# Performance work log

Hardware: AMD Instinct MI355X
Metric: run time of the kernel (lower is better)

Reference implementation:

```python
import jax, jax.numpy as jnp
import numpy as np

N_NODES = 50000
N_EDGES = 800000
D_IN, D_HID, D_OUT = 64, 128, 64


def _glorot(key, fan_in, fan_out):
    lim = (6.0 / (fan_in + fan_out)) ** 0.5
    return jax.random.uniform(key, (fan_in, fan_out), jnp.float32, -lim, lim)


def setup_inputs() -> dict:
    key = jax.random.key(0)
    ks = jax.random.split(key, 10)
    x = jax.random.normal(ks[0], (N_NODES, D_IN), jnp.float32)
    edge_index = jax.random.randint(ks[1], (2, N_EDGES), 0, N_NODES, jnp.int64)
    # GINConv1 MLP: Linear(D_IN->D_HID), ReLU, Linear(D_HID->D_HID)
    W1a = _glorot(ks[2], D_IN, D_HID); b1a = jnp.zeros((D_HID,), jnp.float32)
    W1b = _glorot(ks[3], D_HID, D_HID); b1b = jnp.zeros((D_HID,), jnp.float32)
    # GINConv2 MLP: Linear(D_HID->D_HID), ReLU, Linear(D_HID->D_OUT)
    W2a = _glorot(ks[4], D_HID, D_HID); b2a = jnp.zeros((D_HID,), jnp.float32)
    W2b = _glorot(ks[5], D_HID, D_OUT); b2b = jnp.zeros((D_OUT,), jnp.float32)
    return {"x": x, "edge_index": edge_index,
            "W1a": W1a, "b1a": b1a, "W1b": W1b, "b1b": b1b,
            "W2a": W2a, "b2a": b2a, "W2b": W2b, "b2b": b2b}


def _gin_conv(x, src, dst, Wa, ba, Wb, bb):
    # GIN aggregation (eps = 0): h_i = x_i + sum_{j in N(i)} x_j
    msgs = x[src]                                   # [E, d] gather
    agg = jax.ops.segment_sum(msgs, dst, num_segments=x.shape[0])  # [N, d]
    h = x + agg
    # 2-layer MLP
    h = jax.nn.relu(h @ Wa + ba)
    return h @ Wb + bb


def reference(x, edge_index, W1a, b1a, W1b, b1b, W2a, b2a, W2b, b2b):
    src, dst = edge_index[0], edge_index[1]
    h = jax.nn.relu(_gin_conv(x, src, dst, W1a, b1a, W1b, b1b))
    h = jax.nn.relu(_gin_conv(h, src, dst, W2a, b2a, W2b, b2b))
    return h
```

## Files before the change

kernel.cpp:

```cpp
#include <hip/hip_runtime.h>

#define N_NODES 50000
#define N_EDGES 800000

typedef __attribute__((ext_vector_type(8))) short short8;
typedef __attribute__((ext_vector_type(4))) float floatx4;

static __device__ __forceinline__ unsigned short f2b(float f) {
    unsigned int u = __float_as_uint(f);
    unsigned int r = u + 0x7fffu + ((u >> 16) & 1u);
    return (unsigned short)(r >> 16);
}
static __device__ __forceinline__ unsigned int pk(float a, float b) {
    return (unsigned)f2b(a) | ((unsigned)f2b(b) << 16);
}
static __device__ __forceinline__ float blo(unsigned int u) {
    return __uint_as_float(u << 16);
}
static __device__ __forceinline__ float bhi(unsigned int u) {
    return __uint_as_float(u & 0xffff0000u);
}

static __device__ __forceinline__ void acc4(float* f, uint4 v0, uint4 v1,
                                            uint4 v2, uint4 v3) {
    f[0] += (blo(v0.x) + blo(v1.x)) + (blo(v2.x) + blo(v3.x));
    f[1] += (bhi(v0.x) + bhi(v1.x)) + (bhi(v2.x) + bhi(v3.x));
    f[2] += (blo(v0.y) + blo(v1.y)) + (blo(v2.y) + blo(v3.y));
    f[3] += (bhi(v0.y) + bhi(v1.y)) + (bhi(v2.y) + bhi(v3.y));
    f[4] += (blo(v0.z) + blo(v1.z)) + (blo(v2.z) + blo(v3.z));
    f[5] += (bhi(v0.z) + bhi(v1.z)) + (bhi(v2.z) + bhi(v3.z));
    f[6] += (blo(v0.w) + blo(v1.w)) + (blo(v2.w) + blo(v3.w));
    f[7] += (bhi(v0.w) + bhi(v1.w)) + (bhi(v2.w) + bhi(v3.w));
}

__global__ void hist_rank_kernel(const int* __restrict__ dst,
                                 int* __restrict__ deg, int* __restrict__ rank,
                                 int n) {
    int i = blockIdx.x * blockDim.x + threadIdx.x;
    if (i < n) rank[i] = atomicAdd(&deg[dst[i]], 1);
}

__global__ __launch_bounds__(1024) void offsets_kernel(
    const int* __restrict__ deg, int* __restrict__ offpd,
    int* __restrict__ gcount, unsigned short* __restrict__ nbr, int n) {
    __shared__ int s[1024];
    __shared__ int base;
    const int tid = threadIdx.x;
    const int i = blockIdx.x * 1024 + tid;
    const int d = (i < n) ? deg[i] : 0;
    const int pd = (d + 3) & ~3;
    s[tid] = pd;
    __syncthreads();
    for (int o = 1; o < 1024; o <<= 1) {
        int t = (tid >= o) ? s[tid - o] : 0;
        __syncthreads();
        s[tid] += t;
        __syncthreads();
    }
    if (tid == 1023) base = atomicAdd(gcount, s[1023]);
    __syncthreads();
    const int excl = base + s[tid] - pd;
    if (i < n) {
        offpd[i] = (excl << 10) | pd;
        for (int k = d; k < pd; ++k) nbr[excl + k] = (unsigned short)N_NODES;
    }
}

__global__ void fill_kernel(const int* __restrict__ src,
                            const int* __restrict__ dst,
                            const int* __restrict__ rank,
                            const int* __restrict__ offpd,
                            unsigned short* __restrict__ nbr, int n) {
    int i = blockIdx.x * blockDim.x + threadIdx.x;
    if (i < n) nbr[(offpd[dst[i]] >> 10) + rank[i]] = (unsigned short)src[i];
}

__global__ __launch_bounds__(256) void prep_kernel(
    const float* __restrict__ W1a, const float* __restrict__ W1b,
    const float* __restrict__ W2a, const float* __restrict__ W2b,
    const float* __restrict__ x, unsigned short* __restrict__ W1aT,
    unsigned short* __restrict__ W1bT, unsigned short* __restrict__ W2aT,
    unsigned short* __restrict__ W2bT, unsigned short* __restrict__ xb,
    unsigned short* __restrict__ h, int* __restrict__ deg,
    int* __restrict__ gcount) {
    int i = blockIdx.x * 256 + threadIdx.x;
    if (i < 8192) {
        int n = i >> 6, k = i & 63;
        W1aT[i] = f2b(W1a[k * 128 + n]);
    } else if (i < 24576) {
        int j = i - 8192, n = j >> 7, k = j & 127;
        W1bT[j] = f2b(W1b[k * 128 + n]);
    } else if (i < 40960) {
        int j = i - 24576, n = j >> 7, k = j & 127;
        W2aT[j] = f2b(W2a[k * 128 + n]);
    } else if (i < 49152) {
        int j = i - 40960, n = j >> 7, k = j & 127;
        W2bT[j] = f2b(W2b[k * 64 + n]);
    } else if (i < 49152 + N_NODES * 16) {
        int j = i - 49152;
        float4 v = ((const float4*)x)[j];
        uint2 o;
        o.x = pk(v.x, v.y);
        o.y = pk(v.z, v.w);
        ((uint2*)xb)[j] = o;
    } else if (i < 49152 + N_NODES * 16 + N_NODES) {
        int j = i - (49152 + N_NODES * 16);
        deg[j] = 0;
        if (j == 0) *gcount = 0;
    } else {
        int j = i - (49152 + N_NODES * 16 + N_NODES);
        uint4 z = {0u, 0u, 0u, 0u};
        if (j < 8)
            ((uint4*)(xb + (size_t)N_NODES * 64))[j] = z;
        else if (j < 24)
            ((uint4*)(h + (size_t)N_NODES * 128))[j - 8] = z;
    }
}

template <int DIN, int DH, int DOUT, bool OUT_BF16>
__global__ __launch_bounds__(256) void gin_fused_kernel(
    const unsigned short* __restrict__ xin, const int* __restrict__ offpd,
    const unsigned short* __restrict__ nbr,
    const unsigned short* __restrict__ WaT, const float* __restrict__ ba,
    const unsigned short* __restrict__ WbT, const float* __restrict__ bb,
    void* __restrict__ outp, int n_rows) {
    constexpr int ROWS = 64;
    constexpr int PASSES = DIN / 32;
    constexpr int RS = DIN / 8;
    constexpr int SA = DIN + 16;
    constexpr int SH = DH + 16;
    __shared__ __attribute__((aligned(16))) unsigned short tA[ROWS * SA];
    __shared__ __attribute__((aligned(16))) unsigned short hidA[ROWS * SH];

    const int tid = threadIdx.x;
    const int row0 = blockIdx.x * ROWS;
    const int grp = tid >> 2;
    const int c = tid & 3;
    const int node = row0 + grp;

    int lo = 0, hi = 0;
    if (node < n_rows) {
        const int v = offpd[node];
        lo = v >> 10;
        hi = lo + (v & 1023);
    }

    for (int q = 0; q < PASSES; ++q) {
        float f[8] = {0.f, 0.f, 0.f, 0.f, 0.f, 0.f, 0.f, 0.f};
        const uint4* xr = (const uint4*)xin + q * 4 + c;
        if (node < n_rows) {
            const uint4 a = xr[(size_t)node * RS];
            f[0] = blo(a.x); f[1] = bhi(a.x);
            f[2] = blo(a.y); f[3] = bhi(a.y);
            f[4] = blo(a.z); f[5] = bhi(a.z);
            f[6] = blo(a.w); f[7] = bhi(a.w);
            int j = lo;
            for (; j + 8 <= hi; j += 8) {
                const uint2 i0 = *(const uint2*)&nbr[j];
                const uint2 i1 = *(const uint2*)&nbr[j + 4];
                const int s0 = i0.x & 0xffff, s1 = i0.x >> 16;
                const int s2 = i0.y & 0xffff, s3 = i0.y >> 16;
                const int s4 = i1.x & 0xffff, s5 = i1.x >> 16;
                const int s6 = i1.y & 0xffff, s7 = i1.y >> 16;
                const uint4 v0 = xr[(size_t)s0 * RS];
                const uint4 v1 = xr[(size_t)s1 * RS];
                const uint4 v2 = xr[(size_t)s2 * RS];
                const uint4 v3 = xr[(size_t)s3 * RS];
                const uint4 v4 = xr[(size_t)s4 * RS];
                const uint4 v5 = xr[(size_t)s5 * RS];
                const uint4 v6 = xr[(size_t)s6 * RS];
                const uint4 v7 = xr[(size_t)s7 * RS];
                acc4(f, v0, v1, v2, v3);
                acc4(f, v4, v5, v6, v7);
            }
            if (j < hi) {
                const uint2 i0 = *(const uint2*)&nbr[j];
                const int s0 = i0.x & 0xffff, s1 = i0.x >> 16;
                const int s2 = i0.y & 0xffff, s3 = i0.y >> 16;
                const uint4 v0 = xr[(size_t)s0 * RS];
                const uint4 v1 = xr[(size_t)s1 * RS];
                const uint4 v2 = xr[(size_t)s2 * RS];
                const uint4 v3 = xr[(size_t)s3 * RS];
                acc4(f, v0, v1, v2, v3);
            }
        }
        uint4 o;
        o.x = pk(f[0], f[1]);
        o.y = pk(f[2], f[3]);
        o.z = pk(f[4], f[5]);
        o.w = pk(f[6], f[7]);
        *(uint4*)&tA[grp * SA + q * 32 + c * 8] = o;
    }
    __syncthreads();

    const int lane = tid & 63;
    const int wv = tid >> 6;
    const int quad = lane >> 4;
    const int l16 = lane & 15;
    const int m0 = wv * 16;

    short8 a1[DIN / 32];
#pragma unroll
    for (int kk = 0; kk < DIN / 32; ++kk)
        a1[kk] = *(const short8*)&tA[(m0 + l16) * SA + kk * 32 + quad * 8];
#pragma unroll
    for (int nt = 0; nt < DH / 16; ++nt) {
        const int col = nt * 16 + l16;
        floatx4 acc = {0.f, 0.f, 0.f, 0.f};
#pragma unroll
        for (int kk = 0; kk < DIN / 32; ++kk) {
            short8 b = *(const short8*)&WaT[col * DIN + kk * 32 + quad * 8];
            acc = __builtin_amdgcn_mfma_f32_16x16x32_bf16(a1[kk], b, acc, 0, 0, 0);
        }
        const float bias = ba[col];
#pragma unroll
        for (int r = 0; r < 4; ++r) {
            const float v = fmaxf(acc[r] + bias, 0.f);
            hidA[(m0 + quad * 4 + r) * SH + col] = f2b(v);
        }
    }

    short8 a2[DH / 32];
#pragma unroll
    for (int kk = 0; kk < DH / 32; ++kk)
        a2[kk] = *(const short8*)&hidA[(m0 + l16) * SH + kk * 32 + quad * 8];
#pragma unroll
    for (int nt = 0; nt < DOUT / 16; ++nt) {
        const int col = nt * 16 + l16;
        floatx4 acc = {0.f, 0.f, 0.f, 0.f};
#pragma unroll
        for (int kk = 0; kk < DH / 32; ++kk) {
            short8 b = *(const short8*)&WbT[col * DH + kk * 32 + quad * 8];
            acc = __builtin_amdgcn_mfma_f32_16x16x32_bf16(a2[kk], b, acc, 0, 0, 0);
        }
        const float bias = bb[col];
#pragma unroll
        for (int r = 0; r < 4; ++r) {
            const float v = fmaxf(acc[r] + bias, 0.f);
            const int grow = row0 + m0 + quad * 4 + r;
            if (grow < n_rows) {
                if (OUT_BF16)
                    ((unsigned short*)outp)[(size_t)grow * DOUT + col] = f2b(v);
                else
                    ((float*)outp)[(size_t)grow * DOUT + col] = v;
            }
        }
    }
}

extern "C" void kernel_launch(void* const* d_in, const int* in_sizes, int n_in,
                              void* d_out, int out_size, void* d_ws,
                              size_t ws_size, hipStream_t stream) {
    const float* x   = (const float*)d_in[0];
    const int*   ei  = (const int*)d_in[1];
    const float* W1a = (const float*)d_in[2];
    const float* b1a = (const float*)d_in[3];
    const float* W1b = (const float*)d_in[4];
    const float* b1b = (const float*)d_in[5];
    const float* W2a = (const float*)d_in[6];
    const float* b2a = (const float*)d_in[7];
    const float* W2b = (const float*)d_in[8];
    const float* b2b = (const float*)d_in[9];
    float* out = (float*)d_out;

    const int* src = ei;
    const int* dst = ei + N_EDGES;

    unsigned short* xb = (unsigned short*)d_ws;
    unsigned short* h  = xb + (size_t)(N_NODES + 1) * 64;
    unsigned short* W1aT = h + (size_t)(N_NODES + 1) * 128;
    unsigned short* W1bT = W1aT + 8192;
    unsigned short* W2aT = W1bT + 16384;
    unsigned short* W2bT = W2aT + 16384;
    int* deg    = (int*)(W2bT + 8192);
    int* offpd  = deg + N_NODES;
    int* gcount = offpd + N_NODES;
    int* rank   = gcount + 64;
    unsigned short* nbr = (unsigned short*)(rank + N_EDGES);

    constexpr int NB = (N_NODES + 1023) / 1024;
    constexpr int PREP_THREADS = 49152 + N_NODES * 16 + N_NODES + 24;

    prep_kernel<<<(PREP_THREADS + 255) / 256, 256, 0, stream>>>(
        W1a, W1b, W2a, W2b, x, W1aT, W1bT, W2aT, W2bT, xb, h, deg, gcount);

    hist_rank_kernel<<<(N_EDGES + 255) / 256, 256, 0, stream>>>(dst, deg, rank,
                                                                N_EDGES);
    offsets_kernel<<<NB, 1024, 0, stream>>>(deg, offpd, gcount, nbr, N_NODES);
    fill_kernel<<<(N_EDGES + 255) / 256, 256, 0, stream>>>(src, dst, rank,
                                                           offpd, nbr, N_EDGES);

    gin_fused_kernel<64, 128, 128, true>
        <<<(N_NODES + 63) / 64, 256, 0, stream>>>(xb, offpd, nbr, W1aT, b1a,
                                                  W1bT, b1b, h, N_NODES);

    gin_fused_kernel<128, 128, 64, false>
        <<<(N_NODES + 63) / 64, 256, 0, stream>>>(h, offpd, nbr, W2aT, b2a,
                                                  W2bT, b2b, out, N_NODES);
}
```

Before: 236.9 us.

## Split gather from MLP and slice feature columns per XCD for L2 locality

Splits each fused GIN layer into a separate gather kernel and an MFMA MLP kernel. The gather kernel maps blocks to XCDs round-robin (blockIdx & 7) so that each XCD handles only one 32-column slice of the feature matrix. The intent is that the randomly gathered rows stay resident in that XCD's private L2 rather than thrashing across the full feature width. In exchange it adds two launches and an intermediate aggregated-feature buffer per layer, which must be written to and read back from global memory.

Measured after the change: 244.9 us. 1.03x slower.

```diff
diff --git a/kernel.cpp b/kernel.cpp
--- a/kernel.cpp
+++ b/kernel.cpp
@@ -117,79 +117,93 @@
     }
 }
 
+template <int DIN, int SLICES>
+__global__ __launch_bounds__(256) void gather_sliced_kernel(
+    const unsigned short* __restrict__ xin, const int* __restrict__ offpd,
+    const unsigned short* __restrict__ nbr, unsigned short* __restrict__ tout,
+    int n_rows, int rb_per_part) {
+    constexpr int RS = DIN / 8;
+    const int b = blockIdx.x;
+    const int xcd = b & 7;
+    const int slice = xcd % SLICES;
+    const int part = xcd / SLICES;
+    const int rb = part * rb_per_part + (b >> 3);
+    const int tid = threadIdx.x;
+    const int grp = tid >> 2;
+    const int c = tid & 3;
+    const int node = rb * 64 + grp;
+    if (node >= n_rows) return;
+
+    const int v = offpd[node];
+    const int lo = v >> 10;
+    const int hi = lo + (v & 1023);
+
+    float f[8];
+    const uint4* xr = (const uint4*)xin + slice * 4 + c;
+    const uint4 a = xr[(size_t)node * RS];
+    f[0] = blo(a.x); f[1] = bhi(a.x);
+    f[2] = blo(a.y); f[3] = bhi(a.y);
+    f[4] = blo(a.z); f[5] = bhi(a.z);
+    f[6] = blo(a.w); f[7] = bhi(a.w);
+    int j = lo;
+    for (; j + 8 <= hi; j += 8) {
+        const uint2 i0 = *(const uint2*)&nbr[j];
+        const uint2 i1 = *(const uint2*)&nbr[j + 4];
+        const int s0 = i0.x & 0xffff, s1 = i0.x >> 16;
+        const int s2 = i0.y & 0xffff, s3 = i0.y >> 16;
+        const int s4 = i1.x & 0xffff, s5 = i1.x >> 16;
+        const int s6 = i1.y & 0xffff, s7 = i1.y >> 16;
+        const uint4 v0 = xr[(size_t)s0 * RS];
+        const uint4 v1 = xr[(size_t)s1 * RS];
+        const uint4 v2 = xr[(size_t)s2 * RS];
+        const uint4 v3 = xr[(size_t)s3 * RS];
+        const uint4 v4 = xr[(size_t)s4 * RS];
+        const uint4 v5 = xr[(size_t)s5 * RS];
+        const uint4 v6 = xr[(size_t)s6 * RS];
+        const uint4 v7 = xr[(size_t)s7 * RS];
+        acc4(f, v0, v1, v2, v3);
+        acc4(f, v4, v5, v6, v7);
+    }
+    if (j < hi) {
+        const uint2 i0 = *(const uint2*)&nbr[j];
+        const int s0 = i0.x & 0xffff, s1 = i0.x >> 16;
+        const int s2 = i0.y & 0xffff, s3 = i0.y >> 16;
+        const uint4 v0 = xr[(size_t)s0 * RS];
+        const uint4 v1 = xr[(size_t)s1 * RS];
+        const uint4 v2 = xr[(size_t)s2 * RS];
+        const uint4 v3 = xr[(size_t)s3 * RS];
+        acc4(f, v0, v1, v2, v3);
+    }
+    uint4 o;
+    o.x = pk(f[0], f[1]);
+    o.y = pk(f[2], f[3]);
+    o.z = pk(f[4], f[5]);
+    o.w = pk(f[6], f[7]);
+    ((uint4*)tout)[(size_t)node * RS + slice * 4 + c] = o;
+}
+
 template <int DIN, int DH, int DOUT, bool OUT_BF16>
-__global__ __launch_bounds__(256) void gin_fused_kernel(
-    const unsigned short* __restrict__ xin, const int* __restrict__ offpd,
-    const unsigned short* __restrict__ nbr,
-    const unsigned short* __restrict__ WaT, const float* __restrict__ ba,
-    const unsigned short* __restrict__ WbT, const float* __restrict__ bb,
-    void* __restrict__ outp, int n_rows) {
-    constexpr int ROWS = 64;
-    constexpr int PASSES = DIN / 32;
-    constexpr int RS = DIN / 8;
+__global__ __launch_bounds__(256) void mlp_mfma_kernel(
+    const unsigned short* __restrict__ t, const unsigned short* __restrict__ WaT,
+    const float* __restrict__ ba, const unsigned short* __restrict__ WbT,
+    const float* __restrict__ bb, void* __restrict__ outp, int n_rows) {
     constexpr int SA = DIN + 16;
     constexpr int SH = DH + 16;
-    __shared__ __attribute__((aligned(16))) unsigned short tA[ROWS * SA];
-    __shared__ __attribute__((aligned(16))) unsigned short hidA[ROWS * SH];
+    __shared__ __attribute__((aligned(16))) unsigned short tA[64 * SA];
+    __shared__ __attribute__((aligned(16))) unsigned short hidA[64 * SH];
 
     const int tid = threadIdx.x;
-    const int row0 = blockIdx.x * ROWS;
-    const int grp = tid >> 2;
-    const int c = tid & 3;
-    const int node = row0 + grp;
-
-    int lo = 0, hi = 0;
-    if (node < n_rows) {
-        const int v = offpd[node];
-        lo = v >> 10;
-        hi = lo + (v & 1023);
-    }
-
-    for (int q = 0; q < PASSES; ++q) {
-        float f[8] = {0.f, 0.f, 0.f, 0.f, 0.f, 0.f, 0.f, 0.f};
-        const uint4* xr = (const uint4*)xin + q * 4 + c;
-        if (node < n_rows) {
-            const uint4 a = xr[(size_t)node * RS];
-            f[0] = blo(a.x); f[1] = bhi(a.x);
-            f[2] = blo(a.y); f[3] = bhi(a.y);
-            f[4] = blo(a.z); f[5] = bhi(a.z);
-            f[6] = blo(a.w); f[7] = bhi(a.w);
-            int j = lo;
-            for (; j + 8 <= hi; j += 8) {
-                const uint2 i0 = *(const uint2*)&nbr[j];
-                const uint2 i1 = *(const uint2*)&nbr[j + 4];
-                const int s0 = i0.x & 0xffff, s1 = i0.x >> 16;
-                const int s2 = i0.y & 0xffff, s3 = i0.y >> 16;
-                const int s4 = i1.x & 0xffff, s5 = i1.x >> 16;
-                const int s6 = i1.y & 0xffff, s7 = i1.y >> 16;
-                const uint4 v0 = xr[(size_t)s0 * RS];
-                const uint4 v1 = xr[(size_t)s1 * RS];
-                const uint4 v2 = xr[(size_t)s2 * RS];
-                const uint4 v3 = xr[(size_t)s3 * RS];
-                const uint4 v4 = xr[(size_t)s4 * RS];
-                const uint4 v5 = xr[(size_t)s5 * RS];
-                const uint4 v6 = xr[(size_t)s6 * RS];
-                const uint4 v7 = xr[(size_t)s7 * RS];
-                acc4(f, v0, v1, v2, v3);
-                acc4(f, v4, v5, v6, v7);
-            }
-            if (j < hi) {
-                const uint2 i0 = *(const uint2*)&nbr[j];
-                const int s0 = i0.x & 0xffff, s1 = i0.x >> 16;
-                const int s2 = i0.y & 0xffff, s3 = i0.y >> 16;
-                const uint4 v0 = xr[(size_t)s0 * RS];
-                const uint4 v1 = xr[(size_t)s1 * RS];
-                const uint4 v2 = xr[(size_t)s2 * RS];
-                const uint4 v3 = xr[(size_t)s3 * RS];
-                acc4(f, v0, v1, v2, v3);
-            }
-        }
-        uint4 o;
-        o.x = pk(f[0], f[1]);
-        o.y = pk(f[2], f[3]);
-        o.z = pk(f[4], f[5]);
-        o.w = pk(f[6], f[7]);
-        *(uint4*)&tA[grp * SA + q * 32 + c * 8] = o;
+    const int row0 = blockIdx.x * 64;
+
+    constexpr int CHUNKS = 64 * DIN / 8;
+    const uint4* tg = (const uint4*)t;
+    for (int i = tid; i < CHUNKS; i += 256) {
+        const int row = i / (DIN / 8);
+        const int cb = i % (DIN / 8);
+        uint4 v = {0u, 0u, 0u, 0u};
+        const int gr = row0 + row;
+        if (gr < n_rows) v = tg[(size_t)gr * (DIN / 8) + cb];
+        *(uint4*)&tA[row * SA + cb * 8] = v;
     }
     __syncthreads();
 
@@ -205,18 +219,18 @@
         a1[kk] = *(const short8*)&tA[(m0 + l16) * SA + kk * 32 + quad * 8];
 #pragma unroll
     for (int nt = 0; nt < DH / 16; ++nt) {
-        const int col = nt * 16 + l16;
         floatx4 acc = {0.f, 0.f, 0.f, 0.f};
 #pragma unroll
         for (int kk = 0; kk < DIN / 32; ++kk) {
-            short8 b = *(const short8*)&WaT[col * DIN + kk * 32 + quad * 8];
+            short8 b =
+                *(const short8*)&WaT[(nt * 16 + l16) * DIN + kk * 32 + quad * 8];
             acc = __builtin_amdgcn_mfma_f32_16x16x32_bf16(a1[kk], b, acc, 0, 0, 0);
         }
-        const float bias = ba[col];
+        const float bias = ba[nt * 16 + l16];
 #pragma unroll
         for (int r = 0; r < 4; ++r) {
             const float v = fmaxf(acc[r] + bias, 0.f);
-            hidA[(m0 + quad * 4 + r) * SH + col] = f2b(v);
+            hidA[(m0 + quad * 4 + r) * SH + nt * 16 + l16] = f2b(v);
         }
     }
 
@@ -226,23 +240,24 @@
         a2[kk] = *(const short8*)&hidA[(m0 + l16) * SH + kk * 32 + quad * 8];
 #pragma unroll
     for (int nt = 0; nt < DOUT / 16; ++nt) {
-        const int col = nt * 16 + l16;
         floatx4 acc = {0.f, 0.f, 0.f, 0.f};
 #pragma unroll
         for (int kk = 0; kk < DH / 32; ++kk) {
-            short8 b = *(const short8*)&WbT[col * DH + kk * 32 + quad * 8];
+            short8 b =
+                *(const short8*)&WbT[(nt * 16 + l16) * DH + kk * 32 + quad * 8];
             acc = __builtin_amdgcn_mfma_f32_16x16x32_bf16(a2[kk], b, acc, 0, 0, 0);
         }
-        const float bias = bb[col];
+        const float bias = bb[nt * 16 + l16];
 #pragma unroll
         for (int r = 0; r < 4; ++r) {
             const float v = fmaxf(acc[r] + bias, 0.f);
             const int grow = row0 + m0 + quad * 4 + r;
             if (grow < n_rows) {
                 if (OUT_BF16)
-                    ((unsigned short*)outp)[(size_t)grow * DOUT + col] = f2b(v);
+                    ((unsigned short*)outp)[(size_t)grow * DOUT + nt * 16 + l16] =
+                        f2b(v);
                 else
-                    ((float*)outp)[(size_t)grow * DOUT + col] = v;
+                    ((float*)outp)[(size_t)grow * DOUT + nt * 16 + l16] = v;
             }
         }
     }
@@ -267,8 +282,10 @@
     const int* dst = ei + N_EDGES;
 
     unsigned short* xb = (unsigned short*)d_ws;
-    unsigned short* h  = xb + (size_t)(N_NODES + 1) * 64;
-    unsigned short* W1aT = h + (size_t)(N_NODES + 1) * 128;
+    unsigned short* t1 = xb + (size_t)(N_NODES + 1) * 64;
+    unsigned short* h  = t1 + (size_t)N_NODES * 64;
+    unsigned short* t2 = h + (size_t)(N_NODES + 1) * 128;
+    unsigned short* W1aT = t2 + (size_t)N_NODES * 128;
     unsigned short* W1bT = W1aT + 8192;
     unsigned short* W2aT = W1bT + 16384;
     unsigned short* W2bT = W2aT + 16384;
@@ -280,6 +297,7 @@
 
     constexpr int NB = (N_NODES + 1023) / 1024;
     constexpr int PREP_THREADS = 49152 + N_NODES * 16 + N_NODES + 24;
+    constexpr int NRB = (N_NODES + 63) / 64;
 
     prep_kernel<<<(PREP_THREADS + 255) / 256, 256, 0, stream>>>(
         W1a, W1b, W2a, W2b, x, W1aT, W1bT, W2aT, W2bT, xb, h, deg, gcount);
@@ -290,11 +308,21 @@
     fill_kernel<<<(N_EDGES + 255) / 256, 256, 0, stream>>>(src, dst, rank,
                                                            offpd, nbr, N_EDGES);
 
-    gin_fused_kernel<64, 128, 128, true>
-        <<<(N_NODES + 63) / 64, 256, 0, stream>>>(xb, offpd, nbr, W1aT, b1a,
-                                                  W1bT, b1b, h, N_NODES);
-
-    gin_fused_kernel<128, 128, 64, false>
-        <<<(N_NODES + 63) / 64, 256, 0, stream>>>(h, offpd, nbr, W2aT, b2a,
-                                                  W2bT, b2b, out, N_NODES);
-}
+    {
+        constexpr int PARTS = 8 / 2;
+        constexpr int RBP = (NRB + PARTS - 1) / PARTS;
+        gather_sliced_kernel<64, 2><<<8 * RBP, 256, 0, stream>>>(
+            xb, offpd, nbr, t1, N_NODES, RBP);
+    }
+    mlp_mfma_kernel<64, 128, 128, true>
+        <<<NRB, 256, 0, stream>>>(t1, W1aT, b1a, W1bT, b1b, h, N_NODES);
+
+    {
+        constexpr int PARTS = 8 / 4;
+        constexpr int RBP = (NRB + PARTS - 1) / PARTS;
+        gather_sliced_kernel<128, 4><<<8 * RBP, 256, 0, stream>>>(
+            h, offpd, nbr, t2, N_NODES, RBP);
+    }
+    mlp_mfma_kernel<128, 128, 64, false>
+        <<<NRB, 256, 0, stream>>>(t2, W2aT, b2a, W2bT, b2b, out, N_NODES);
+}
```
